# Kernel tuning notes

Measured on AMD Instinct MI355X. Metric: run time of the kernel, lower is better.

The kernel has to match this reference:

```python
import jax, jax.numpy as jnp
import numpy as np

B, N1, R12, R23 = 1, 4096, 4, 4
N2, N3 = N1 * R12, N1 * R12 * R23
D, F, H, NCLS, K = 1024, 512, 256, 4, 256


def setup_inputs() -> dict:
    key = jax.random.key(0)
    ks = jax.random.split(key, 10)
    s = 0.02
    return {
        "x1": jax.random.normal(ks[0], (B, N1, D), jnp.float32),
        "x2": jax.random.normal(ks[1], (B, N2, D), jnp.float32),
        "x3": jax.random.normal(ks[2], (B, N3, D), jnp.float32),
        # 3 fc layers (low/mid/high mag): Linear(D->F)
        "fcW": (jax.random.normal(ks[3], (3, D, F), jnp.float32) * s),
        "fcb": jnp.zeros((3, F), jnp.float32),
        # 5 gated-attention modules: 0=ga_low,1=ga_mid,2=ga_high,3=aux_low,4=aux_mid
        "gaWa": (jax.random.normal(ks[4], (5, F, H), jnp.float32) * s),
        "gaba": jnp.zeros((5, H), jnp.float32),
        "gaWb": (jax.random.normal(ks[5], (5, F, H), jnp.float32) * s),
        "gabb": jnp.zeros((5, H), jnp.float32),
        "gaWc": (jax.random.normal(ks[6], (5, H, 1), jnp.float32) * s),
        "gabc": jnp.zeros((5, 1), jnp.float32),
        "Wh": (jax.random.normal(ks[7], (F, NCLS), jnp.float32) * s),
        "bh": jnp.zeros((NCLS,), jnp.float32),
        "k_sample": K,
    }


def _ga(x, i, Wa, ba, Wb, bb, Wc, bc):
    # GatedAttention: tanh branch * sigmoid branch -> Linear(H->1); returns (B,N)
    a = jnp.tanh(x @ Wa[i] + ba[i])
    g = jax.nn.sigmoid(x @ Wb[i] + bb[i])
    return ((a * g) @ Wc[i] + bc[i])[..., 0]


def _block_gather(x, idx, ratio):
    # Equivalent to einsum('bkn,bnd->bkd', kron(one_hot(idx), eye(ratio)), x):
    # pick contiguous blocks of `ratio` rows for each selected coarse index.
    b, n, d = x.shape
    xb = x.reshape(b, n // ratio, ratio, d)
    out = jnp.take_along_axis(xb, idx[:, :, None, None], axis=1)  # (B,k,ratio,D)
    return out.reshape(b, idx.shape[1] * ratio, d)


def reference(x1, x2, x3, fcW, fcb, gaWa, gaba, gaWb, gabb, gaWc, gabc, Wh, bh, k_sample):
    ga = (gaWa, gaba, gaWb, gabb, gaWc, gabc)
    n1, n2, n3 = x1.shape[1], x2.shape[1], x3.shape[1]

    # --- low mag ---
    h1 = jax.nn.relu(x1 @ fcW[0] + fcb[0])                    # (B,N1,F)
    A1 = jax.nn.softmax(_ga(h1, 0, *ga), axis=-1)             # (B,N1)
    M1 = jnp.einsum('bn,bnf->bf', A1, h1)                     # (B,F)
    A1_aux = jax.nn.softmax(_ga(h1, 3, *ga), axis=-1)
    k1 = min(n1, int(k_sample))
    idx1 = jnp.sort(jax.lax.top_k(A1_aux, k1)[1], axis=-1)    # (B,k1)

    # zoom: gather selected blocks from mid and high mag features
    x2s = _block_gather(x2, idx1, n2 // n1)                   # (B,k1*R12,D)
    x3s = _block_gather(x3, idx1, n3 // n1)                   # (B,k1*R12*R23,D)

    # --- mid mag ---
    h2 = jax.nn.relu(x2s @ fcW[1] + fcb[1])
    A2 = jax.nn.softmax(_ga(h2, 1, *ga), axis=-1)
    M2 = jnp.einsum('bn,bnf->bf', A2, h2)
    A2_aux = jax.nn.softmax(_ga(h2, 4, *ga), axis=-1)
    k2 = min(h2.shape[1], int(k_sample))
    idx2 = jnp.sort(jax.lax.top_k(A2_aux, k2)[1], axis=-1)

    x3s2 = _block_gather(x3s, idx2, n3 // n2)                 # (B,k2*R23,D)

    # --- high mag ---
    h3 = jax.nn.relu(x3s2 @ fcW[2] + fcb[2])
    A3 = jax.nn.softmax(_ga(h3, 2, *ga), axis=-1)
    M3 = jnp.einsum('bn,bnf->bf', A3, h3)

    M = M1 + M2 + M3                                           # (B,F)
    logits = M @ Wh + bh                                       # (B,NCLS)
    return logits
```

## Files before the change

### kernel.cpp

```cpp
#include <hip/hip_runtime.h>
#include <hip/hip_bf16.h>
#include <math.h>


typedef __attribute__((ext_vector_type(8))) short short8;
typedef __attribute__((ext_vector_type(4))) float float4a;

__device__ __forceinline__ ushort f2bf(float f) {
    unsigned u = __float_as_uint(f);
    return (ushort)((u + 0x7fffu + ((u >> 16) & 1u)) >> 16);
}
__device__ __forceinline__ uint pk2(float a, float b) {
    __hip_bfloat162 t = __float22bfloat162_rn(make_float2(a, b));
    uint u; __builtin_memcpy(&u, &t, 4); return u;
}
__device__ __forceinline__ float aload(const float* p) {
    return __hip_atomic_load(p, __ATOMIC_RELAXED, __HIP_MEMORY_SCOPE_AGENT);
}

template<int SPLIT, int ABF>
__global__ __launch_bounds__(256) void zm_hgemm(
    const void* __restrict__ Av, int lda,
    const int* __restrict__ rowmap,
    const ushort* __restrict__ Bt,
    const float* __restrict__ bias,
    float* __restrict__ Cf, ushort* __restrict__ Cb, int ldc, int K)
{
    __shared__ ushort As[64 * 40];
    __shared__ ushort Bs[64 * 40];
    const int tid = threadIdx.x;
    const int brow = blockIdx.y << 6;
    const int bcol = blockIdx.x << 6;
    const int kbeg = SPLIT ? ((int)blockIdx.z << 8) : 0;
    const int kend = SPLIT ? kbeg + 256 : K;

    const int sr = tid >> 2;
    const int sk = (tid & 3) << 3;
    int arow = brow + sr;
    if (rowmap) arow = rowmap[arow];
    const float*  Apf = (const float*)Av + (size_t)arow * lda;
    const ushort* Apb = (const ushort*)Av + (size_t)arow * lda;
    const ushort* Bp = Bt + (size_t)(bcol + sr) * K + sk;

    const int w = tid >> 6;
    const int wm = (w >> 1) << 5;
    const int wn = (w & 1) << 5;
    const int lane = tid & 63;
    const int lm = lane & 15;
    const int lq = lane >> 4;

    float4a acc[2][2] = {};

    for (int k0 = kbeg; k0 < kend; k0 += 32) {
        if (ABF) {
            *(uint4*)&As[sr * 40 + sk] = *(const uint4*)(Apb + k0 + sk);
        } else {
            const float* ap = Apf + k0 + sk;
            float4 v0 = *(const float4*)(ap);
            float4 v1 = *(const float4*)(ap + 4);
            uint4 p0;
            p0.x = pk2(v0.x, v0.y); p0.y = pk2(v0.z, v0.w);
            p0.z = pk2(v1.x, v1.y); p0.w = pk2(v1.z, v1.w);
            *(uint4*)&As[sr * 40 + sk] = p0;
        }
        *(uint4*)&Bs[sr * 40 + sk] = *(const uint4*)(Bp + k0);
        __syncthreads();
        short8 afr[2], bfr[2];
#pragma unroll
        for (int mt = 0; mt < 2; mt++)
            afr[mt] = *(const short8*)&As[(wm + mt * 16 + lm) * 40 + lq * 8];
#pragma unroll
        for (int nt = 0; nt < 2; nt++)
            bfr[nt] = *(const short8*)&Bs[(wn + nt * 16 + lm) * 40 + lq * 8];
#pragma unroll
        for (int mt = 0; mt < 2; mt++)
#pragma unroll
            for (int nt = 0; nt < 2; nt++)
                acc[mt][nt] = __builtin_amdgcn_mfma_f32_16x16x32_bf16(
                    afr[mt], bfr[nt], acc[mt][nt], 0, 0, 0);
        __syncthreads();
    }

#pragma unroll
    for (int mt = 0; mt < 2; mt++) {
#pragma unroll
        for (int nt = 0; nt < 2; nt++) {
            int gc = bcol + wn + nt * 16 + lm;
            float bv = bias[gc];
            if (SPLIT && blockIdx.z != 0) bv = 0.0f;
#pragma unroll
            for (int r = 0; r < 4; r++) {
                int gr = brow + wm + mt * 16 + lq * 4 + r;
                float v = acc[mt][nt][r] + bv;
                if (SPLIT) {
                    atomicAdd(&Cf[(size_t)gr * ldc + gc], v);
                } else {
                    v = fmaxf(v, 0.0f);
                    Cf[(size_t)gr * ldc + gc] = v;
                    Cb[(size_t)gr * ldc + gc] = f2bf(v);
                }
            }
        }
    }
}

template<int AMODE>
__global__ __launch_bounds__(256) void zm_sgemm(
    const void* __restrict__ Av, int lda,
    const ushort* __restrict__ Bt,
    const float* __restrict__ bint,
    const float* __restrict__ wc0, const float* __restrict__ wc1,
    float* __restrict__ sMain, float* __restrict__ sAux,
    float* __restrict__ statsOut, int* __restrict__ cnt2, int lastBlk)
{
    __shared__ ushort As[64 * 40];
    __shared__ ushort Bs[64 * 40];
    __shared__ float part[4][64];
    const int tid = threadIdx.x;
    const int brow = blockIdx.y << 6;
    const int bcol = blockIdx.x << 6;

    const int sr = tid >> 2;
    const int sk = (tid & 3) << 3;
    const float*  Af = (const float*)Av;
    const ushort* Ab = (const ushort*)Av;
    const ushort* Bp = Bt + (size_t)(bcol + sr) * 512 + sk;

    const int w = tid >> 6;
    const int wn = w << 4;
    const int lane = tid & 63;
    const int lm = lane & 15;
    const int lq = lane >> 4;

    float4a acc[4] = {};

    for (int k0 = 0; k0 < 512; k0 += 32) {
        if (AMODE == 0) {
            *(uint4*)&As[sr * 40 + sk] =
                *(const uint4*)(Ab + (size_t)(brow + sr) * lda + k0 + sk);
        } else {
            const float* ap = Af + (size_t)(brow + sr) * lda + k0 + sk;
            float4 v0 = *(const float4*)ap;
            float4 v1 = *(const float4*)(ap + 4);
            v0.x = fmaxf(v0.x, 0.f); v0.y = fmaxf(v0.y, 0.f);
            v0.z = fmaxf(v0.z, 0.f); v0.w = fmaxf(v0.w, 0.f);
            v1.x = fmaxf(v1.x, 0.f); v1.y = fmaxf(v1.y, 0.f);
            v1.z = fmaxf(v1.z, 0.f); v1.w = fmaxf(v1.w, 0.f);
            uint4 pk;
            pk.x = pk2(v0.x, v0.y); pk.y = pk2(v0.z, v0.w);
            pk.z = pk2(v1.x, v1.y); pk.w = pk2(v1.z, v1.w);
            *(uint4*)&As[sr * 40 + sk] = pk;
        }
        *(uint4*)&Bs[sr * 40 + sk] = *(const uint4*)(Bp + k0);
        __syncthreads();
        short8 bfr = *(const short8*)&Bs[(wn + lm) * 40 + lq * 8];
#pragma unroll
        for (int mt = 0; mt < 4; mt++) {
            short8 afr = *(const short8*)&As[(mt * 16 + lm) * 40 + lq * 8];
            acc[mt] = __builtin_amdgcn_mfma_f32_16x16x32_bf16(afr, bfr, acc[mt], 0, 0, 0);
        }
        __syncthreads();
    }

    const int gc = bcol + wn + lm;
    const float* wcp = (gc >= 512) ? wc1 : wc0;
    const float wcv = wcp[(gc & 511) >> 1];
    const float bv = bint[gc];
    const bool odd = (gc & 1);
    float* sp = (bcol >= 512) ? sAux : sMain;

#pragma unroll
    for (int mt = 0; mt < 4; mt++) {
        float red[4];
#pragma unroll
        for (int r = 0; r < 4; r++) {
            float v = acc[mt][r] + bv;
            float x = odd ? (1.0f / (1.0f + expf(-v))) : tanhf(v);
            float prt = __shfl_xor(x, 1);
            float ctr = odd ? 0.0f : (x * prt * wcv);
            ctr += __shfl_xor(ctr, 1);
            ctr += __shfl_xor(ctr, 2);
            ctr += __shfl_xor(ctr, 4);
            ctr += __shfl_xor(ctr, 8);
            red[r] = ctr;
        }
        if (lm == 0) {
#pragma unroll
            for (int r = 0; r < 4; r++) part[w][mt * 16 + lq * 4 + r] = red[r];
        }
    }
    __syncthreads();
    if (tid < 64) {
        float tot = part[0][tid] + part[1][tid] + part[2][tid] + part[3][tid];
        atomicAdd(&sp[brow + tid], tot);
    }

    if (statsOut) {
        __threadfence();
        __shared__ int lastf;
        if (tid == 0)
            lastf = (__hip_atomic_fetch_add(cnt2, 1, __ATOMIC_ACQ_REL,
                                            __HIP_MEMORY_SCOPE_AGENT) == lastBlk);
        __syncthreads();
        if (lastf) {
            float* red = (float*)part;
            float vv[4];
            float mx = -3.4e38f;
#pragma unroll
            for (int j = 0; j < 4; j++) {
                vv[j] = aload(&sMain[tid + j * 256]);
                mx = fmaxf(mx, vv[j]);
            }
            red[tid] = mx; __syncthreads();
            for (int o = 128; o > 0; o >>= 1) {
                if (tid < o) red[tid] = fmaxf(red[tid], red[tid + o]);
                __syncthreads();
            }
            mx = red[0]; __syncthreads();
            float z = 0.0f;
#pragma unroll
            for (int j = 0; j < 4; j++) z += expf(vv[j] - mx);
            red[tid] = z; __syncthreads();
            for (int o = 128; o > 0; o >>= 1) {
                if (tid < o) red[tid] += red[tid + o];
                __syncthreads();
            }
            if (tid == 0) { statsOut[0] = mx; statsOut[1] = red[0]; }
        }
    }
}

__global__ __launch_bounds__(1024) void zm_topk(
    const float* __restrict__ sa, const float* __restrict__ sm, int n,
    const int* __restrict__ idx_prev,
    int* __restrict__ idx_out, int* __restrict__ rm_out,
    float* __restrict__ stOut)
{
    __shared__ float redf[1024];
    __shared__ int hist[2048];
    __shared__ unsigned ckey[4096];
    __shared__ int cidx[4096];
    __shared__ int idxbuf[256];
    __shared__ int wsum[16];
    __shared__ int bc[4];
    __shared__ unsigned bcT;
    const int bs = 1024;
    const int tid = threadIdx.x;

    if (blockIdx.x == 1) {
        float mx = -3.4e38f;
        for (int i = tid; i < n; i += bs) mx = fmaxf(mx, sm[i]);
        redf[tid] = mx; __syncthreads();
        for (int o = 512; o > 0; o >>= 1) {
            if (tid < o) redf[tid] = fmaxf(redf[tid], redf[tid + o]);
            __syncthreads();
        }
        mx = redf[0]; __syncthreads();
        float z = 0.0f;
        for (int i = tid; i < n; i += bs) z += expf(sm[i] - mx);
        redf[tid] = z; __syncthreads();
        for (int o = 512; o > 0; o >>= 1) {
            if (tid < o) redf[tid] += redf[tid + o];
            __syncthreads();
        }
        if (tid == 0) { stOut[0] = mx; stOut[1] = redf[0]; }
        return;
    }

    const int ept = n >> 10;
    const int lane = tid & 63;
    unsigned key[4];
#pragma unroll
    for (int e = 0; e < 4; e++) key[e] = 0;
    for (int e = 0; e < ept; e++) {
        unsigned u = __float_as_uint(sa[tid * ept + e]);
        key[e] = (u & 0x80000000u) ? ~u : (u | 0x80000000u);
    }

    int need = 256;
    int c = 0;
    for (int level = 0; level < 3; level++) {
        const int shift = (level == 0) ? 21 : ((level == 1) ? 10 : 0);
        hist[tid] = 0; hist[tid + 1024] = 0;
        if (tid == 0) bc[2] = 0;
        __syncthreads();
        if (level == 0) {
            for (int e = 0; e < ept; e++) atomicAdd(&hist[key[e] >> 21], 1);
        } else {
            for (int j = tid; j < c; j += bs)
                atomicAdd(&hist[(ckey[j] >> shift) & 2047], 1);
        }
        __syncthreads();
        int h0 = hist[2 * tid], h1 = hist[2 * tid + 1];
        int q = h0 + h1;
        int suf = q;
#pragma unroll
        for (int o = 1; o < 64; o <<= 1) {
            int v = __shfl_down(suf, o);
            if (lane + o < 64) suf += v;
        }
        if (lane == 0) wsum[tid >> 6] = suf;
        __syncthreads();
        if (tid < 16) {
            int v = wsum[tid];
            int s = v;
#pragma unroll
            for (int o = 1; o < 16; o <<= 1) {
                int t2 = __shfl_down(s, o);
                if (tid + o < 16) s += t2;
            }
            wsum[tid] = s - v;
        }
        __syncthreads();
        int abv1 = wsum[tid >> 6] + (suf - q);
        int abv0 = abv1 + h1;
        if (abv1 < need && abv1 + h1 >= need) { bc[0] = 2 * tid + 1; bc[1] = abv1; }
        if (abv0 < need && abv0 + h0 >= need) { bc[0] = 2 * tid;     bc[1] = abv0; }
        __syncthreads();
        const int B = bc[0];
        const int above = bc[1];
        if (level == 0) {
            for (int e = 0; e < ept; e++)
                if ((int)(key[e] >> 21) == B) {
                    int s2 = atomicAdd(&bc[2], 1);
                    ckey[s2] = key[e]; cidx[s2] = tid * ept + e;
                }
            __syncthreads();
        } else {
            unsigned rk[4]; int ri[4]; int rc = 0;
            for (int j = tid; j < c; j += bs)
                if ((int)((ckey[j] >> shift) & 2047) == B) {
                    rk[rc] = ckey[j]; ri[rc] = cidx[j]; rc++;
                }
            __syncthreads();
            for (int qq = 0; qq < rc; qq++) {
                int s2 = atomicAdd(&bc[2], 1);
                ckey[s2] = rk[qq]; cidx[s2] = ri[qq];
            }
            __syncthreads();
        }
        c = bc[2];
        need -= above;
        if (c <= 256 || level == 2) break;
    }

    if (tid == 0) bc[3] = 0;
    __syncthreads();
    for (int j = tid; j < c; j += bs) {
        unsigned kj = ckey[j]; int ij = cidx[j];
        int rank = 0;
        for (int i = 0; i < c; i++) {
            unsigned ki = ckey[i];
            rank += (ki > kj) || (ki == kj && cidx[i] < ij);
        }
        if (rank == need - 1) bcT = kj;
    }
    __syncthreads();
    const unsigned T = bcT;
    for (int j = tid; j < c; j += bs)
        if (ckey[j] > T) atomicAdd(&bc[3], 1);
    __syncthreads();
    const int m = need - bc[3];

    int gt = 0, eq = 0;
    for (int e = 0; e < ept; e++) { gt += (key[e] > T); eq += (key[e] == T); }
    int packed = (gt << 16) | eq;
    int incl = packed;
#pragma unroll
    for (int o = 1; o < 64; o <<= 1) {
        int v = __shfl_up(incl, o);
        if (lane >= o) incl += v;
    }
    if (lane == 63) wsum[tid >> 6] = incl;
    __syncthreads();
    if (tid < 64) {
        int v = (tid < 16) ? wsum[tid] : 0;
        int s = v;
#pragma unroll
        for (int o = 1; o < 16; o <<= 1) {
            int t2 = __shfl_up(s, o);
            if (tid >= o) s += t2;
        }
        if (tid < 16) wsum[tid] = s - v;
    }
    __syncthreads();
    int base = wsum[tid >> 6] + incl - packed;
    int gt_before = base >> 16;
    int eq_before = base & 0xffff;
    for (int e = 0; e < ept; e++) {
        if (key[e] > T) {
            int eqa = (eq_before < m) ? eq_before : m;
            idxbuf[gt_before + eqa] = tid * ept + e;
            gt_before++;
        } else if (key[e] == T) {
            if (eq_before < m) idxbuf[gt_before + eq_before] = tid * ept + e;
            eq_before++;
        }
    }
    __syncthreads();
    if (tid < 256) idx_out[tid] = idxbuf[tid];
    int t = idxbuf[tid >> 2] * 4 + (tid & 3);
    rm_out[tid] = idx_prev ? (idx_prev[t >> 4] * 16 + (t & 15)) : t;
}

__global__ __launch_bounds__(256) void zm_prep(
    const float* __restrict__ fcW,
    const float* __restrict__ gaWa, const float* __restrict__ gaWb,
    const float* __restrict__ gaba, const float* __restrict__ gabb,
    ushort* __restrict__ fc_t, ushort* __restrict__ gint,
    float* __restrict__ bint, float4* __restrict__ zbase, int zn4,
    const float* __restrict__ x1, ushort* __restrict__ x1b)
{
    const int b = blockIdx.x;
    const int tid = threadIdx.x;
    if (b >= 2881) {
        const int base = ((b - 2881) * 256 + tid) * 8;
        for (int it = 0; it < 8; it++) {
            int i = base + it * 524288;
            float4 a = *(const float4*)(x1 + i);
            float4 b4 = *(const float4*)(x1 + i + 4);
            uint4 o;
            o.x = pk2(a.x, a.y); o.y = pk2(a.z, a.w);
            o.z = pk2(b4.x, b4.y); o.w = pk2(b4.z, b4.w);
            *(uint4*)(x1b + i) = o;
        }
        return;
    }
    if (b >= 2817) {
        float4 z4 = make_float4(0.f, 0.f, 0.f, 0.f);
        for (int i = (b - 2817) * 256 + tid; i < zn4; i += 64 * 256)
            zbase[i] = z4;
        return;
    }
    if (b == 2816) {
        for (int i = tid; i < 2560; i += 256) {
            int n, head;
            if (i < 1024)      { n = i;        head = (n >> 9) ? 3 : 0; }
            else if (i < 2048) { n = i - 1024; head = (n >> 9) ? 4 : 1; }
            else               { n = i - 2048; head = 2; }
            int h = (n & 511) >> 1;
            const float* src = (n & 1) ? gabb : gaba;
            bint[i] = src[head * 256 + h];
        }
        return;
    }
    __shared__ ushort tile[32][33];
    const int c = tid & 31, r8 = tid >> 5;
    if (b < 1536) {
        int mat = b >> 9, rem = b & 511;
        int tk = rem >> 4, tn = rem & 15;
        const float* src = fcW + (size_t)mat * 1024 * 512;
        ushort* dst = fc_t + (size_t)mat * 512 * 1024;
        int k0 = tk * 32, n0 = tn * 32;
#pragma unroll
        for (int it = 0; it < 4; it++) {
            int r = r8 + it * 8;
            tile[r][c] = f2bf(src[(size_t)(k0 + r) * 512 + n0 + c]);
        }
        __syncthreads();
#pragma unroll
        for (int it = 0; it < 4; it++) {
            int r = r8 + it * 8;
            dst[(size_t)(n0 + r) * 1024 + k0 + c] = tile[c][r];
        }
    } else {
        int idx = b - 1536;
        int mat = idx >> 7, rem = idx & 127;
        int tk = rem >> 3, th = rem & 7;
        int head = mat >> 1, br = mat & 1;
        const float* src = (br ? gaWb : gaWa) + (size_t)head * 512 * 256;
        ushort* dstb; int off;
        if (head == 0)      { dstb = gint;              off = 0;   }
        else if (head == 1) { dstb = gint + 1024 * 512; off = 0;   }
        else if (head == 2) { dstb = gint + 2048 * 512; off = 0;   }
        else if (head == 3) { dstb = gint;              off = 512; }
        else                { dstb = gint + 1024 * 512; off = 512; }
        int k0 = tk * 32, h0 = th * 32;
#pragma unroll
        for (int it = 0; it < 4; it++) {
            int r = r8 + it * 8;
            tile[r][c] = f2bf(src[(size_t)(k0 + r) * 256 + h0 + c]);
        }
        __syncthreads();
#pragma unroll
        for (int it = 0; it < 4; it++) {
            int r = r8 + it * 8;
            dstb[(size_t)(off + 2 * (h0 + r) + br) * 512 + k0 + c] = tile[c][r];
        }
    }
}

__global__ __launch_bounds__(256) void zm_final(
    const float* __restrict__ h1f, const float* __restrict__ h2f,
    const float* __restrict__ h3f,
    const float* __restrict__ s1, const float* __restrict__ s2,
    const float* __restrict__ s3,
    const float* __restrict__ st, float* __restrict__ Mbuf,
    int* __restrict__ cnt,
    const float* __restrict__ Wh, const float* __restrict__ bh,
    float* __restrict__ out)
{
    const int tid = threadIdx.x;
    const int b = blockIdx.x;
    const float* h; const float* s; const float* stp; int r0, rl;
    if (b < 64)      { h = h1f; s = s1; stp = st;     r0 = b * 64;        rl = 0; }
    else if (b < 80) { h = h2f; s = s2; stp = st + 2; r0 = (b - 64) * 64; rl = 1; }
    else             { h = h3f; s = s3; stp = st + 4; r0 = (b - 80) * 64; rl = 1; }
    const float mx = stp[0];
    const float invZ = 1.0f / stp[1];
    float a0 = 0.0f, a1 = 0.0f;
    for (int r = 0; r < 64; r++) {
        int n = r0 + r;
        float wgt = expf(s[n] - mx) * invZ;
        float v0 = h[(size_t)n * 512 + tid];
        float v1 = h[(size_t)n * 512 + 256 + tid];
        if (rl) { v0 = fmaxf(v0, 0.f); v1 = fmaxf(v1, 0.f); }
        a0 += wgt * v0; a1 += wgt * v1;
    }
    atomicAdd(&Mbuf[tid], a0);
    atomicAdd(&Mbuf[tid + 256], a1);
    __threadfence();
    __shared__ int lastf;
    if (tid == 0)
        lastf = (__hip_atomic_fetch_add(cnt, 1, __ATOMIC_ACQ_REL,
                                        __HIP_MEMORY_SCOPE_AGENT) == 95);
    __syncthreads();
    if (lastf) {
        const int c = tid >> 6, lane = tid & 63;
        float pacc = 0.0f;
        for (int f = lane; f < 512; f += 64)
            pacc += aload(&Mbuf[f]) * Wh[f * 4 + c];
        for (int o = 32; o > 0; o >>= 1) pacc += __shfl_down(pacc, o);
        if (lane == 0) out[c] = pacc + bh[c];
    }
}

extern "C" void kernel_launch(void* const* d_in, const int* in_sizes, int n_in,
                              void* d_out, int out_size, void* d_ws, size_t ws_size,
                              hipStream_t stream)
{
    const float* x1   = (const float*)d_in[0];
    const float* x2   = (const float*)d_in[1];
    const float* x3   = (const float*)d_in[2];
    const float* fcW  = (const float*)d_in[3];
    const float* fcb  = (const float*)d_in[4];
    const float* gaWa = (const float*)d_in[5];
    const float* gaba = (const float*)d_in[6];
    const float* gaWb = (const float*)d_in[7];
    const float* gabb = (const float*)d_in[8];
    const float* gaWc = (const float*)d_in[9];
    const float* Wh   = (const float*)d_in[11];
    const float* bh   = (const float*)d_in[12];
    float* out = (float*)d_out;

    char* p = (char*)d_ws;
    float*  h1f  = (float*)p;
    ushort* h1b  = (ushort*)(p + 8388608);
    ushort* fc_t = (ushort*)(p + 12582912);
    ushort* gint = (ushort*)(p + 15728640);
    float*  bint = (float*)(p + 18350080);
    float*  st   = (float*)(p + 18360320);
    int*    idx1 = (int*)(p + 18360352);
    int*    idx2 = (int*)(p + 18361376);
    int*    rm2  = (int*)(p + 18362400);
    int*    rm3  = (int*)(p + 18366496);
    char*   zbase = p + 18370592;
    float*  h2f  = (float*)zbase;
    float*  h3f  = (float*)(zbase + 2097152);
    float*  s1   = (float*)(zbase + 4194304);
    float*  s1a  = (float*)(zbase + 4210688);
    float*  s2   = (float*)(zbase + 4227072);
    float*  s2a  = (float*)(zbase + 4231168);
    float*  s3   = (float*)(zbase + 4235264);
    float*  Mbuf = (float*)(zbase + 4239360);
    int*    cnt  = (int*)(zbase + 4241408);
    const int ZN4 = 4241424 / 16;
    ushort* x1b  = (ushort*)(p + 22612032);

    zm_prep<<<3137, 256, 0, stream>>>(fcW, gaWa, gaWb, gaba, gabb,
                                      fc_t, gint, bint, (float4*)zbase, ZN4,
                                      x1, x1b);
    zm_hgemm<0, 1><<<dim3(8, 64), 256, 0, stream>>>(x1b, 1024, nullptr, fc_t,
                                                    fcb, h1f, h1b, 512, 1024);
    zm_sgemm<0><<<dim3(16, 64), 256, 0, stream>>>(h1b, 512, gint, bint,
                                                  gaWc, gaWc + 3 * 256,
                                                  s1, s1a, nullptr, nullptr, 0);
    zm_topk<<<2, 1024, 0, stream>>>(s1a, s1, 4096, nullptr, idx1, rm2, st);
    zm_hgemm<1, 0><<<dim3(8, 16, 4), 256, 0, stream>>>(x2, 1024, rm2,
                                                       fc_t + 512 * 1024,
                                                       fcb + 512,
                                                       h2f, nullptr, 512, 1024);
    zm_sgemm<1><<<dim3(16, 16), 256, 0, stream>>>(h2f, 512, gint + 1024 * 512,
                                                  bint + 1024,
                                                  gaWc + 256, gaWc + 4 * 256,
                                                  s2, s2a, nullptr, nullptr, 0);
    zm_topk<<<2, 1024, 0, stream>>>(s2a, s2, 1024, idx1, idx2, rm3, st + 2);
    zm_hgemm<1, 0><<<dim3(8, 16, 4), 256, 0, stream>>>(x3, 1024, rm3,
                                                       fc_t + 2 * 512 * 1024,
                                                       fcb + 1024,
                                                       h3f, nullptr, 512, 1024);
    zm_sgemm<1><<<dim3(8, 16), 256, 0, stream>>>(h3f, 512, gint + 2048 * 512,
                                                 bint + 2048,
                                                 gaWc + 2 * 256, gaWc + 2 * 256,
                                                 s3, s3, st + 4, cnt + 1, 127);
    zm_final<<<96, 256, 0, stream>>>(h1f, h2f, h3f, s1, s2, s3, st, Mbuf, cnt,
                                     Wh, bh, out);
}
```

Measured before the change: 527.0 us.

## Replace split-K atomics with two partial buffers summed in consumers

The split-K gathered GEMMs for mid and high magnification now use 2 K-splits with 32-row tiles, and write each split's partial result to its own buffer instead of atomically adding into a zeroed output. The downstream attention GEMM and final pooling read both partial buffers, add them and apply ReLU. This drops the float atomics and most of the zero-fill work in the prep kernel. In exchange the consumers read twice the data, and the smaller M tile lowers operand reuse per block.

```diff
diff --git a/kernel.cpp b/kernel.cpp
--- a/kernel.cpp
+++ b/kernel.cpp
@@ -26,54 +26,64 @@
     const float* __restrict__ bias,
     float* __restrict__ Cf, ushort* __restrict__ Cb, int ldc, int K)
 {
-    __shared__ ushort As[64 * 40];
+    constexpr int BM = SPLIT ? 32 : 64;
+    constexpr int MT = SPLIT ? 1 : 2;
+    __shared__ ushort As[BM * 40];
     __shared__ ushort Bs[64 * 40];
     const int tid = threadIdx.x;
-    const int brow = blockIdx.y << 6;
+    const int brow = blockIdx.y * BM;
     const int bcol = blockIdx.x << 6;
-    const int kbeg = SPLIT ? ((int)blockIdx.z << 8) : 0;
-    const int kend = SPLIT ? kbeg + 256 : K;
-
-    const int sr = tid >> 2;
-    const int sk = (tid & 3) << 3;
-    int arow = brow + sr;
+    const int kbeg = SPLIT ? ((int)blockIdx.z << 9) : 0;
+    const int kend = SPLIT ? kbeg + 512 : K;
+
+    const int asr = SPLIT ? (tid >> 3) : (tid >> 2);
+    const int ask = SPLIT ? ((tid & 7) << 2) : ((tid & 3) << 3);
+    int arow = brow + asr;
     if (rowmap) arow = rowmap[arow];
     const float*  Apf = (const float*)Av + (size_t)arow * lda;
     const ushort* Apb = (const ushort*)Av + (size_t)arow * lda;
-    const ushort* Bp = Bt + (size_t)(bcol + sr) * K + sk;
+
+    const int bsr = tid >> 2;
+    const int bsk = (tid & 3) << 3;
+    const ushort* Bp = Bt + (size_t)(bcol + bsr) * K + bsk;
 
     const int w = tid >> 6;
-    const int wm = (w >> 1) << 5;
+    const int wm = (w >> 1) << (SPLIT ? 4 : 5);
     const int wn = (w & 1) << 5;
     const int lane = tid & 63;
     const int lm = lane & 15;
     const int lq = lane >> 4;
 
-    float4a acc[2][2] = {};
+    float4a acc[MT][2] = {};
 
     for (int k0 = kbeg; k0 < kend; k0 += 32) {
         if (ABF) {
-            *(uint4*)&As[sr * 40 + sk] = *(const uint4*)(Apb + k0 + sk);
+            *(uint4*)&As[asr * 40 + ask] = *(const uint4*)(Apb + k0 + ask);
+        } else if (SPLIT) {
+            float4 v0 = *(const float4*)(Apf + k0 + ask);
+            uint2 p;
+            p.x = pk2(v0.x, v0.y); p.y = pk2(v0.z, v0.w);
+            *(uint2*)&As[asr * 40 + ask] = p;
         } else {
-            const float* ap = Apf + k0 + sk;
+            const float* ap = Apf + k0 + ask;
             float4 v0 = *(const float4*)(ap);
             float4 v1 = *(const float4*)(ap + 4);
             uint4 p0;
             p0.x = pk2(v0.x, v0.y); p0.y = pk2(v0.z, v0.w);
             p0.z = pk2(v1.x, v1.y); p0.w = pk2(v1.z, v1.w);
-            *(uint4*)&As[sr * 40 + sk] = p0;
-        }
-        *(uint4*)&Bs[sr * 40 + sk] = *(const uint4*)(Bp + k0);
-        __syncthreads();
-        short8 afr[2], bfr[2];
-#pragma unroll
-        for (int mt = 0; mt < 2; mt++)
+            *(uint4*)&As[asr * 40 + ask] = p0;
+        }
+        *(uint4*)&Bs[bsr * 40 + bsk] = *(const uint4*)(Bp + k0);
+        __syncthreads();
+        short8 afr[MT], bfr[2];
+#pragma unroll
+        for (int mt = 0; mt < MT; mt++)
             afr[mt] = *(const short8*)&As[(wm + mt * 16 + lm) * 40 + lq * 8];
 #pragma unroll
         for (int nt = 0; nt < 2; nt++)
             bfr[nt] = *(const short8*)&Bs[(wn + nt * 16 + lm) * 40 + lq * 8];
 #pragma unroll
-        for (int mt = 0; mt < 2; mt++)
+        for (int mt = 0; mt < MT; mt++)
 #pragma unroll
             for (int nt = 0; nt < 2; nt++)
                 acc[mt][nt] = __builtin_amdgcn_mfma_f32_16x16x32_bf16(
@@ -81,8 +91,10 @@
         __syncthreads();
     }
 
-#pragma unroll
-    for (int mt = 0; mt < 2; mt++) {
+    const size_t zoff = SPLIT
+        ? (size_t)blockIdx.z * ((size_t)gridDim.y * BM * ldc) : 0;
+#pragma unroll
+    for (int mt = 0; mt < MT; mt++) {
 #pragma unroll
         for (int nt = 0; nt < 2; nt++) {
             int gc = bcol + wn + nt * 16 + lm;
@@ -93,7 +105,7 @@
                 int gr = brow + wm + mt * 16 + lq * 4 + r;
                 float v = acc[mt][nt][r] + bv;
                 if (SPLIT) {
-                    atomicAdd(&Cf[(size_t)gr * ldc + gc], v);
+                    Cf[zoff + (size_t)gr * ldc + gc] = v;
                 } else {
                     v = fmaxf(v, 0.0f);
                     Cf[(size_t)gr * ldc + gc] = v;
@@ -140,15 +152,17 @@
                 *(const uint4*)(Ab + (size_t)(brow + sr) * lda + k0 + sk);
         } else {
             const float* ap = Af + (size_t)(brow + sr) * lda + k0 + sk;
-            float4 v0 = *(const float4*)ap;
-            float4 v1 = *(const float4*)(ap + 4);
-            v0.x = fmaxf(v0.x, 0.f); v0.y = fmaxf(v0.y, 0.f);
-            v0.z = fmaxf(v0.z, 0.f); v0.w = fmaxf(v0.w, 0.f);
-            v1.x = fmaxf(v1.x, 0.f); v1.y = fmaxf(v1.y, 0.f);
-            v1.z = fmaxf(v1.z, 0.f); v1.w = fmaxf(v1.w, 0.f);
+            float4 a0 = *(const float4*)ap;
+            float4 a1 = *(const float4*)(ap + 4);
+            float4 b0 = *(const float4*)(ap + 524288);
+            float4 b1 = *(const float4*)(ap + 524292);
+            a0.x = fmaxf(a0.x + b0.x, 0.f); a0.y = fmaxf(a0.y + b0.y, 0.f);
+            a0.z = fmaxf(a0.z + b0.z, 0.f); a0.w = fmaxf(a0.w + b0.w, 0.f);
+            a1.x = fmaxf(a1.x + b1.x, 0.f); a1.y = fmaxf(a1.y + b1.y, 0.f);
+            a1.z = fmaxf(a1.z + b1.z, 0.f); a1.w = fmaxf(a1.w + b1.w, 0.f);
             uint4 pk;
-            pk.x = pk2(v0.x, v0.y); pk.y = pk2(v0.z, v0.w);
-            pk.z = pk2(v1.x, v1.y); pk.w = pk2(v1.z, v1.w);
+            pk.x = pk2(a0.x, a0.y); pk.y = pk2(a0.z, a0.w);
+            pk.z = pk2(a1.x, a1.y); pk.w = pk2(a1.z, a1.w);
             *(uint4*)&As[sr * 40 + sk] = pk;
         }
         *(uint4*)&Bs[sr * 40 + sk] = *(const uint4*)(Bp + k0);
@@ -413,8 +427,8 @@
 {
     const int b = blockIdx.x;
     const int tid = threadIdx.x;
-    if (b >= 2881) {
-        const int base = ((b - 2881) * 256 + tid) * 8;
+    if (b >= 2821) {
+        const int base = ((b - 2821) * 256 + tid) * 8;
         for (int it = 0; it < 8; it++) {
             int i = base + it * 524288;
             float4 a = *(const float4*)(x1 + i);
@@ -428,7 +442,7 @@
     }
     if (b >= 2817) {
         float4 z4 = make_float4(0.f, 0.f, 0.f, 0.f);
-        for (int i = (b - 2817) * 256 + tid; i < zn4; i += 64 * 256)
+        for (int i = (b - 2817) * 256 + tid; i < zn4; i += 4 * 256)
             zbase[i] = z4;
         return;
     }
@@ -512,9 +526,16 @@
     for (int r = 0; r < 64; r++) {
         int n = r0 + r;
         float wgt = expf(s[n] - mx) * invZ;
-        float v0 = h[(size_t)n * 512 + tid];
-        float v1 = h[(size_t)n * 512 + 256 + tid];
-        if (rl) { v0 = fmaxf(v0, 0.f); v1 = fmaxf(v1, 0.f); }
+        float v0, v1;
+        if (rl) {
+            v0 = fmaxf(h[(size_t)n * 512 + tid] +
+                       h[(size_t)n * 512 + tid + 524288], 0.f);
+            v1 = fmaxf(h[(size_t)n * 512 + 256 + tid] +
+                       h[(size_t)n * 512 + 256 + tid + 524288], 0.f);
+        } else {
+            v0 = h[(size_t)n * 512 + tid];
+            v1 = h[(size_t)n * 512 + 256 + tid];
+        }
         a0 += wgt * v0; a1 += wgt * v1;
     }
     atomicAdd(&Mbuf[tid], a0);
@@ -565,19 +586,19 @@
     int*    rm2  = (int*)(p + 18362400);
     int*    rm3  = (int*)(p + 18366496);
     char*   zbase = p + 18370592;
-    float*  h2f  = (float*)zbase;
-    float*  h3f  = (float*)(zbase + 2097152);
-    float*  s1   = (float*)(zbase + 4194304);
-    float*  s1a  = (float*)(zbase + 4210688);
-    float*  s2   = (float*)(zbase + 4227072);
-    float*  s2a  = (float*)(zbase + 4231168);
-    float*  s3   = (float*)(zbase + 4235264);
-    float*  Mbuf = (float*)(zbase + 4239360);
-    int*    cnt  = (int*)(zbase + 4241408);
-    const int ZN4 = 4241424 / 16;
-    ushort* x1b  = (ushort*)(p + 22612032);
-
-    zm_prep<<<3137, 256, 0, stream>>>(fcW, gaWa, gaWb, gaba, gabb,
+    float*  s1   = (float*)zbase;
+    float*  s1a  = (float*)(zbase + 16384);
+    float*  s2   = (float*)(zbase + 32768);
+    float*  s2a  = (float*)(zbase + 36864);
+    float*  s3   = (float*)(zbase + 40960);
+    float*  Mbuf = (float*)(zbase + 45056);
+    int*    cnt  = (int*)(zbase + 47104);
+    const int ZN4 = 47120 / 16;
+    float*  h2f  = (float*)(p + 18417728);
+    float*  h3f  = (float*)(p + 22612032);
+    ushort* x1b  = (ushort*)(p + 26806336);
+
+    zm_prep<<<3077, 256, 0, stream>>>(fcW, gaWa, gaWb, gaba, gabb,
                                       fc_t, gint, bint, (float4*)zbase, ZN4,
                                       x1, x1b);
     zm_hgemm<0, 1><<<dim3(8, 64), 256, 0, stream>>>(x1b, 1024, nullptr, fc_t,
@@ -586,20 +607,20 @@
                                                   gaWc, gaWc + 3 * 256,
                                                   s1, s1a, nullptr, nullptr, 0);
     zm_topk<<<2, 1024, 0, stream>>>(s1a, s1, 4096, nullptr, idx1, rm2, st);
-    zm_hgemm<1, 0><<<dim3(8, 16, 4), 256, 0, stream>>>(x2, 1024, rm2,
+    zm_hgemm<1, 0><<<dim3(8, 32, 2), 256, 0, stream>>>(x2, 1024, rm2,
                                                        fc_t + 512 * 1024,
                                                        fcb + 512,
                                                        h2f, nullptr, 512, 1024);
-    zm_sgemm<1><<<dim3(16, 16), 256, 0, stream>>>(h2f, 512, gint + 1024 * 512,
+    zm_sgemm<2><<<dim3(16, 16), 256, 0, stream>>>(h2f, 512, gint + 1024 * 512,
                                                   bint + 1024,
                                                   gaWc + 256, gaWc + 4 * 256,
                                                   s2, s2a, nullptr, nullptr, 0);
     zm_topk<<<2, 1024, 0, stream>>>(s2a, s2, 1024, idx1, idx2, rm3, st + 2);
-    zm_hgemm<1, 0><<<dim3(8, 16, 4), 256, 0, stream>>>(x3, 1024, rm3,
+    zm_hgemm<1, 0><<<dim3(8, 32, 2), 256, 0, stream>>>(x3, 1024, rm3,
                                                        fc_t + 2 * 512 * 1024,
                                                        fcb + 1024,
                                                        h3f, nullptr, 512, 1024);
-    zm_sgemm<1><<<dim3(8, 16), 256, 0, stream>>>(h3f, 512, gint + 2048 * 512,
+    zm_sgemm<2><<<dim3(8, 16), 256, 0, stream>>>(h3f, 512, gint + 2048 * 512,
                                                  bint + 2048,
                                                  gaWc + 2 * 256, gaWc + 2 * 256,
                                                  s3, s3, st + 4, cnt + 1, 127);
```

Measured after the change: 528.2 us. About the same (+0.2%).
